# Kernel optimization log

Hardware: AMD Instinct MI355X
Metric: run time of the kernel (lower is better)

## Reference

```python
import jax, jax.numpy as jnp
import numpy as np

B, T, NQ, NK = 2, 8, 128, 128
DIM_IN, DIM_OUT = 64, 256


def setup_inputs() -> dict:
    key = jax.random.key(0)
    ks = jax.random.split(key, 6)
    scale = 0.05  # keep tanh out of full saturation
    return {
        "query": jax.random.normal(ks[0], (B, NQ, DIM_IN), dtype=jnp.float32),
        "keys": jax.random.normal(ks[1], (B, T, NK, DIM_IN), dtype=jnp.float32),
        "Wq": jax.random.normal(ks[2], (DIM_IN, DIM_OUT), dtype=jnp.float32) * scale,
        "Wk": jax.random.normal(ks[3], (DIM_IN, DIM_OUT), dtype=jnp.float32) * scale,
        "bk": jax.random.normal(ks[4], (DIM_OUT,), dtype=jnp.float32) * scale,
        "v": jax.random.normal(ks[5], (DIM_OUT,), dtype=jnp.float32) * scale,
    }


def reference(query, keys, Wq, Wk, bk, v):
    # q: [B, Nq, D], k: [B, T, Nk, D]
    q = jnp.einsum("bqi,id->bqd", query, Wq)
    k = jnp.einsum("btki,id->btkd", keys, Wk) + bk
    # broadcast add -> [B, T, Nq, Nk, D], tanh, then score projection D->1
    h = jnp.tanh(q[:, None, :, None, :] + k[:, :, None, :, :])
    scores = jnp.einsum("btqkd,d->btqk", h, v)
    return jax.nn.softmax(scores, axis=-1)
```

## Files before the change

kernel.cpp:

```cpp
#include <hip/hip_runtime.h>

#define C_TANH 2.8853900817779268f

__global__ __launch_bounds__(256) void proj_kernel(
    const float* __restrict__ query, const float* __restrict__ keys,
    const float* __restrict__ Wq, const float* __restrict__ Wk,
    const float* __restrict__ bk, float* __restrict__ q1,
    float* __restrict__ k2) {
  int bid = blockIdx.x;
  int d   = threadIdx.x;
  if (bid < 256) {
    int bt = bid >> 4;
    int kg = bid & 15;
    __shared__ float4 krows4[128];
    if (threadIdx.x < 128)
      krows4[threadIdx.x] =
          ((const float4*)(keys + bt * 8192 + kg * 512))[threadIdx.x];
    __syncthreads();

    float acc[8];
    float bias = bk[d];
#pragma unroll
    for (int kk = 0; kk < 8; ++kk) acc[kk] = bias;
#pragma unroll 4
    for (int i4 = 0; i4 < 16; ++i4) {
      float wa = Wk[(i4 * 4 + 0) * 256 + d];
      float wb = Wk[(i4 * 4 + 1) * 256 + d];
      float wc = Wk[(i4 * 4 + 2) * 256 + d];
      float wd = Wk[(i4 * 4 + 3) * 256 + d];
#pragma unroll
      for (int kk = 0; kk < 8; ++kk) {
        float4 kr = krows4[kk * 16 + i4];
        acc[kk] = fmaf(kr.x, wa, acc[kk]);
        acc[kk] = fmaf(kr.y, wb, acc[kk]);
        acc[kk] = fmaf(kr.z, wc, acc[kk]);
        acc[kk] = fmaf(kr.w, wd, acc[kk]);
      }
    }
#pragma unroll
    for (int kk = 0; kk < 8; ++kk)
      k2[(bt * 256 + d) * 128 + kg * 8 + kk] = acc[kk] * C_TANH;
  } else {
    int row = bid - 256;
    __shared__ float qrow[64];
    if (threadIdx.x < 64) qrow[threadIdx.x] = query[row * 64 + threadIdx.x];
    __syncthreads();
    float acc = 0.f;
#pragma unroll
    for (int i = 0; i < 64; ++i) acc += qrow[i] * Wq[i * 256 + d];
    q1[row * 256 + d] = acc * C_TANH;
  }
}

__global__ __launch_bounds__(256) void score_kernel(
    const float* __restrict__ q1, const float* __restrict__ v,
    const float* __restrict__ k2, float* __restrict__ out) {
  __shared__ float2 qv[4][256];
  int tid = threadIdx.x;
  int r   = tid >> 6;
  int kk  = tid & 63;
  int g0  = blockIdx.x * 4;
  int bt  = g0 >> 7;
  int b   = g0 >> 10;
  int q1base = b * 128 + (g0 & 127);

  for (int idx = tid; idx < 1024; idx += 256) {
    int rr = idx >> 8;
    int d  = idx & 255;
    qv[rr][d] = make_float2(q1[(q1base + rr) * 256 + d], v[d]);
  }
  __syncthreads();

  const float2* kp2 = (const float2*)(k2 + bt * 32768) + kk;
  float acc0 = 0.f, acc1 = 0.f;
#pragma unroll 8
  for (int d = 0; d < 256; ++d) {
    float2 qvv = qv[r][d];
    float2 kv  = kp2[d * 64];
    float x0 = qvv.x + kv.x;
    float x1 = qvv.x + kv.y;
    float e0 = __builtin_amdgcn_exp2f(x0);
    float e1 = __builtin_amdgcn_exp2f(x1);
    float r0 = __builtin_amdgcn_rcpf(1.0f + e0);
    float r1 = __builtin_amdgcn_rcpf(1.0f + e1);
    acc0 = fmaf(qvv.y, r0, acc0);
    acc1 = fmaf(qvv.y, r1, acc1);
  }
  float s0 = -C_TANH * acc0;
  float s1 = -C_TANH * acc1;

  float m = fmaxf(s0, s1);
#pragma unroll
  for (int off = 32; off > 0; off >>= 1) m = fmaxf(m, __shfl_xor(m, off, 64));
  float e0 = __builtin_amdgcn_exp2f(s0 - m);
  float e1 = __builtin_amdgcn_exp2f(s1 - m);
  float ssum = e0 + e1;
#pragma unroll
  for (int off = 32; off > 0; off >>= 1) ssum += __shfl_xor(ssum, off, 64);
  float inv = __builtin_amdgcn_rcpf(ssum);

  ((float2*)(out + (g0 + r) * 128))[kk] = make_float2(e0 * inv, e1 * inv);
}

extern "C" void kernel_launch(void* const* d_in, const int* in_sizes, int n_in,
                              void* d_out, int out_size, void* d_ws, size_t ws_size,
                              hipStream_t stream) {
  const float* query = (const float*)d_in[0];
  const float* keys  = (const float*)d_in[1];
  const float* Wq    = (const float*)d_in[2];
  const float* Wk    = (const float*)d_in[3];
  const float* bk    = (const float*)d_in[4];
  const float* v     = (const float*)d_in[5];
  float* out = (float*)d_out;

  float* ws = (float*)d_ws;
  float* q1 = ws;
  float* k2 = ws + 65536;

  proj_kernel<<<512, 256, 0, stream>>>(query, keys, Wq, Wk, bk, q1, k2);
  score_kernel<<<512, 256, 0, stream>>>(q1, v, k2, out);
}
```

Measured before the change: 89.13 us.

## Use tanh addition identity with precomputed tanh of projections and LDS-staged keys

Precomputes tanh of the q and k projections in the projection kernel, then evaluates tanh(a+b) in the score loop as (ta+tb)/(1+ta*tb). This replaces an exp2 plus reciprocal per element with one FMA plus one reciprocal. The score kernel also stages the transposed key projection tile through LDS in four chunks and adds an occupancy hint. The identity can lose accuracy near saturation (ta*tb close to -1), and the extra LDS staging brings more barriers.

Result: no change. 88.20 us (-1.0%).

```diff
diff --git a/kernel.cpp b/kernel.cpp
--- a/kernel.cpp
+++ b/kernel.cpp
@@ -1,12 +1,18 @@
 #include <hip/hip_runtime.h>
 
 #define C_TANH 2.8853900817779268f
+#define LOG2E  1.4426950408889634f
+
+__device__ __forceinline__ float tanh_exact(float x) {
+  float e = __builtin_amdgcn_exp2f(C_TANH * x);
+  return 1.0f - 2.0f * __builtin_amdgcn_rcpf(1.0f + e);
+}
 
 __global__ __launch_bounds__(256) void proj_kernel(
     const float* __restrict__ query, const float* __restrict__ keys,
     const float* __restrict__ Wq, const float* __restrict__ Wk,
-    const float* __restrict__ bk, float* __restrict__ q1,
-    float* __restrict__ k2) {
+    const float* __restrict__ bk, float* __restrict__ q1t,
+    float* __restrict__ k2t) {
   int bid = blockIdx.x;
   int d   = threadIdx.x;
   if (bid < 256) {
@@ -17,7 +23,6 @@
       krows4[threadIdx.x] =
           ((const float4*)(keys + bt * 8192 + kg * 512))[threadIdx.x];
     __syncthreads();
-
     float acc[8];
     float bias = bk[d];
 #pragma unroll
@@ -39,7 +44,7 @@
     }
 #pragma unroll
     for (int kk = 0; kk < 8; ++kk)
-      k2[(bt * 256 + d) * 128 + kg * 8 + kk] = acc[kk] * C_TANH;
+      k2t[(bt * 256 + d) * 128 + kg * 8 + kk] = tanh_exact(acc[kk]);
   } else {
     int row = bid - 256;
     __shared__ float qrow[64];
@@ -48,47 +53,58 @@
     float acc = 0.f;
 #pragma unroll
     for (int i = 0; i < 64; ++i) acc += qrow[i] * Wq[i * 256 + d];
-    q1[row * 256 + d] = acc * C_TANH;
+    q1t[row * 256 + d] = tanh_exact(acc);
   }
 }
 
-__global__ __launch_bounds__(256) void score_kernel(
-    const float* __restrict__ q1, const float* __restrict__ v,
-    const float* __restrict__ k2, float* __restrict__ out) {
-  __shared__ float2 qv[4][256];
+__global__ __launch_bounds__(256, 4) void score_kernel(
+    const float* __restrict__ q1t, const float* __restrict__ v,
+    const float* __restrict__ k2t, float* __restrict__ out) {
+  __shared__ float  tb[64 * 128];
+  __shared__ float2 qv[4 * 256];
   int tid = threadIdx.x;
-  int r   = tid >> 6;
+  int wid = tid >> 6;
   int kk  = tid & 63;
-  int g0  = blockIdx.x * 4;
-  int bt  = g0 >> 7;
-  int b   = g0 >> 10;
-  int q1base = b * 128 + (g0 & 127);
+  int blk = blockIdx.x;
+  int bt  = blk >> 5;
+  int qg  = blk & 31;
+  int b   = bt >> 3;
+  int q0  = qg * 4;
 
-  for (int idx = tid; idx < 1024; idx += 256) {
-    int rr = idx >> 8;
-    int d  = idx & 255;
-    qv[rr][d] = make_float2(q1[(q1base + rr) * 256 + d], v[d]);
+  for (int i = tid; i < 1024; i += 256) {
+    int rr = i >> 8;
+    int d  = i & 255;
+    qv[i] = make_float2(q1t[(b * 128 + q0 + rr) * 256 + d], v[d] * LOG2E);
   }
-  __syncthreads();
 
-  const float2* kp2 = (const float2*)(k2 + bt * 32768) + kk;
-  float acc0 = 0.f, acc1 = 0.f;
+  const float* ksrc = k2t + bt * 32768;
+  float2 acc = make_float2(0.f, 0.f);
+
+#pragma unroll
+  for (int h = 0; h < 4; ++h) {
+    __syncthreads();
+    const float4* src4 = (const float4*)(ksrc + h * 8192);
+    float4* dst4 = (float4*)tb;
+    for (int i = tid; i < 2048; i += 256) dst4[i] = src4[i];
+    __syncthreads();
+
+    const float2* tb2 = (const float2*)tb;
 #pragma unroll 8
-  for (int d = 0; d < 256; ++d) {
-    float2 qvv = qv[r][d];
-    float2 kv  = kp2[d * 64];
-    float x0 = qvv.x + kv.x;
-    float x1 = qvv.x + kv.y;
-    float e0 = __builtin_amdgcn_exp2f(x0);
-    float e1 = __builtin_amdgcn_exp2f(x1);
-    float r0 = __builtin_amdgcn_rcpf(1.0f + e0);
-    float r1 = __builtin_amdgcn_rcpf(1.0f + e1);
-    acc0 = fmaf(qvv.y, r0, acc0);
-    acc1 = fmaf(qvv.y, r1, acc1);
+    for (int d = 0; d < 64; ++d) {
+      float2 tav = qv[wid * 256 + h * 64 + d];
+      float2 tbv = tb2[d * 64 + kk];
+      float n0 = tav.x + tbv.x;
+      float n1 = tav.x + tbv.y;
+      float d0 = fmaf(tav.x, tbv.x, 1.0f);
+      float d1 = fmaf(tav.x, tbv.y, 1.0f);
+      float r0 = n0 * __builtin_amdgcn_rcpf(d0);
+      float r1 = n1 * __builtin_amdgcn_rcpf(d1);
+      acc.x = fmaf(tav.y, r0, acc.x);
+      acc.y = fmaf(tav.y, r1, acc.y);
+    }
   }
-  float s0 = -C_TANH * acc0;
-  float s1 = -C_TANH * acc1;
 
+  float s0 = acc.x, s1 = acc.y;
   float m = fmaxf(s0, s1);
 #pragma unroll
   for (int off = 32; off > 0; off >>= 1) m = fmaxf(m, __shfl_xor(m, off, 64));
@@ -99,7 +115,8 @@
   for (int off = 32; off > 0; off >>= 1) ssum += __shfl_xor(ssum, off, 64);
   float inv = __builtin_amdgcn_rcpf(ssum);
 
-  ((float2*)(out + (g0 + r) * 128))[kk] = make_float2(e0 * inv, e1 * inv);
+  int row = bt * 128 + q0 + wid;
+  ((float2*)(out + row * 128))[kk] = make_float2(e0 * inv, e1 * inv);
 }
 
 extern "C" void kernel_launch(void* const* d_in, const int* in_sizes, int n_in,
@@ -113,10 +130,10 @@
   const float* v     = (const float*)d_in[5];
   float* out = (float*)d_out;
 
-  float* ws = (float*)d_ws;
-  float* q1 = ws;
-  float* k2 = ws + 65536;
+  float* ws  = (float*)d_ws;
+  float* q1t = ws;
+  float* k2t = ws + 65536;
 
-  proj_kernel<<<512, 256, 0, stream>>>(query, keys, Wq, Wk, bk, q1, k2);
-  score_kernel<<<512, 256, 0, stream>>>(q1, v, k2, out);
+  proj_kernel<<<512, 256, 0, stream>>>(query, keys, Wq, Wk, bk, q1t, k2t);
+  score_kernel<<<512, 256, 0, stream>>>(q1t, v, k2t, out);
 }
```
